# Performance work log

Hardware: AMD Instinct MI355X
Metric: run time of the kernel (lower is better)

The kernel has to match this reference:

```python
import jax, jax.numpy as jnp
import numpy as np

NEG = -1e9  # masked-out (non-edge) additive bias


def _attn_head(seq, bias_mat, W1, a1, b1, a2, b2, W2, bW):
    # seq: [B,N,F]; W1: [F,H]; a1,a2: [H]; W2: [H,K]
    fts = jnp.einsum('bnf,fh->bnh', seq, W1)            # Conv1D(out_sz,1,no bias)
    f1 = jnp.einsum('bnh,h->bn', fts, a1) + b1          # Conv1D(1,1)
    f2 = jnp.einsum('bnh,h->bn', fts, a2) + b2          # Conv1D(1,1)
    logits = f1[:, :, None] + f2[:, None, :]            # [B,N,N] additive attention
    coefs = jax.nn.softmax(jax.nn.leaky_relu(logits, 0.2) + bias_mat, axis=-1)
    vals = jnp.einsum('bnm,bmh->bnh', coefs, fts)       # weighted aggregation
    return jnp.einsum('bnh,hk->bnk', vals, W2) + bW     # bias_add_layer1 (Dense)


def setup_inputs() -> dict:
    B, N, F, H, NH, C = 1, 4096, 512, 64, 8, 40
    key = jax.random.key(0)
    ks = jax.random.split(key, 12)
    seq = jax.random.normal(ks[0], (B, N, F), dtype=jnp.float32)
    adj = jax.random.bernoulli(ks[1], 0.01, (B, N, N)) | jnp.eye(N, dtype=bool)[None]
    bias_mat = jnp.where(adj, 0.0, NEG).astype(jnp.float32)
    s = 0.05
    # 8 stacked first-layer heads (out_sz=H)
    W1 = jax.random.normal(ks[2], (NH, F, H), dtype=jnp.float32) * s
    a1 = jax.random.normal(ks[3], (NH, H), dtype=jnp.float32) * s
    b1 = jnp.zeros((NH,), jnp.float32)
    a2 = jax.random.normal(ks[4], (NH, H), dtype=jnp.float32) * s
    b2 = jnp.zeros((NH,), jnp.float32)
    W2 = jax.random.normal(ks[5], (NH, H, H), dtype=jnp.float32) * s
    bW = jnp.zeros((NH, H), jnp.float32)
    # single output head (out_sz=nb_classes, identity activation)
    Wo1 = jax.random.normal(ks[6], (NH * H, C), dtype=jnp.float32) * s
    ao1 = jax.random.normal(ks[7], (C,), dtype=jnp.float32) * s
    bo1 = jnp.zeros((), jnp.float32)
    ao2 = jax.random.normal(ks[8], (C,), dtype=jnp.float32) * s
    bo2 = jnp.zeros((), jnp.float32)
    Wo2 = jax.random.normal(ks[9], (C, C), dtype=jnp.float32) * s
    bo = jnp.zeros((C,), jnp.float32)
    return dict(seq=seq, bias_mat=bias_mat, W1=W1, a1=a1, b1=b1, a2=a2, b2=b2,
                W2=W2, bW=bW, Wo1=Wo1, ao1=ao1, bo1=bo1, ao2=ao2, bo2=bo2,
                Wo2=Wo2, bo=bo)


def reference(seq, bias_mat, W1, a1, b1, a2, b2, W2, bW,
              Wo1, ao1, bo1, ao2, bo2, Wo2, bo):
    # first layer: 8 heads with elu activation, vmapped over head params
    heads = jax.vmap(
        lambda w1, v1, c1, v2, c2, w2, bw: jax.nn.elu(
            _attn_head(seq, bias_mat, w1, v1, c1, v2, c2, w2, bw))
    )(W1, a1, b1, a2, b2, W2, bW)                        # [NH,B,N,H]
    NH, B, N, H = heads.shape
    h1 = jnp.moveaxis(heads, 0, 2).reshape(B, N, NH * H)  # concat along features
    # output layer: 1 head, identity activation, averaged over n_heads[-1]=1
    out = _attn_head(h1, bias_mat, Wo1, ao1, bo1, ao2, bo2, Wo2, bo)
    return out / 1.0
```

## Files before the change

### kernel.cpp

```cpp
#include <hip/hip_runtime.h>
#include <cstdint>
#include <cstddef>

#define NN 4096
#define FDIM 512
#define HDIM 64
#define NHEAD 8
#define CDIM 40
#define MAXD 256

typedef __attribute__((ext_vector_type(8))) short bf16x8;
typedef __attribute__((ext_vector_type(16))) float f32x16;

__device__ __forceinline__ float wave_max64(float v) {
  for (int o = 32; o; o >>= 1) v = fmaxf(v, __shfl_xor(v, o));
  return v;
}
__device__ __forceinline__ float wave_sum64(float v) {
  for (int o = 32; o; o >>= 1) v += __shfl_xor(v, o);
  return v;
}
__device__ __forceinline__ float readlane_f(float v, int sl) {
  return __uint_as_float((unsigned)__builtin_amdgcn_readlane((int)__float_as_uint(v), sl));
}
__device__ __forceinline__ int readlane_i(int v, int sl) {
  return __builtin_amdgcn_readlane(v, sl);
}
__device__ __forceinline__ unsigned short f2bf(float x) {
  unsigned u = __float_as_uint(x);
  return (unsigned short)((u + 0x7fffu + ((u >> 16) & 1u)) >> 16);
}
__device__ __forceinline__ float bf2f(unsigned short b) {
  return __uint_as_float(((unsigned)b) << 16);
}
__device__ __forceinline__ float lo16f(int u) { return __int_as_float(u << 16); }
__device__ __forceinline__ float hi16f(int u) { return __int_as_float(u & 0xffff0000); }
__device__ __forceinline__ void cvt8(const float4& a, const float4& b,
                                     int4& hi, int4& lo) {
  unsigned short h0 = f2bf(a.x), h1 = f2bf(a.y), h2 = f2bf(a.z), h3 = f2bf(a.w);
  unsigned short h4 = f2bf(b.x), h5 = f2bf(b.y), h6 = f2bf(b.z), h7 = f2bf(b.w);
  hi = make_int4((int)((unsigned)h0 | ((unsigned)h1 << 16)),
                 (int)((unsigned)h2 | ((unsigned)h3 << 16)),
                 (int)((unsigned)h4 | ((unsigned)h5 << 16)),
                 (int)((unsigned)h6 | ((unsigned)h7 << 16)));
  unsigned short l0 = f2bf(a.x - bf2f(h0)), l1 = f2bf(a.y - bf2f(h1));
  unsigned short l2 = f2bf(a.z - bf2f(h2)), l3 = f2bf(a.w - bf2f(h3));
  unsigned short l4 = f2bf(b.x - bf2f(h4)), l5 = f2bf(b.y - bf2f(h5));
  unsigned short l6 = f2bf(b.z - bf2f(h6)), l7 = f2bf(b.w - bf2f(h7));
  lo = make_int4((int)((unsigned)l0 | ((unsigned)l1 << 16)),
                 (int)((unsigned)l2 | ((unsigned)l3 << 16)),
                 (int)((unsigned)l4 | ((unsigned)l5 << 16)),
                 (int)((unsigned)l6 | ((unsigned)l7 << 16)));
}

__global__ __launch_bounds__(256) void k_prep(
    const float* __restrict__ W1, short* __restrict__ Bhi, short* __restrict__ Blo,
    const float* __restrict__ W2, short* __restrict__ W2thi, short* __restrict__ W2tlo,
    const float* __restrict__ Wo1, short* __restrict__ Wo1thi, short* __restrict__ Wo1tlo) {
  __shared__ float T[64][65];
  int bx = blockIdx.x, tid = threadIdx.x;
  if (bx < 64) {
    int h = bx >> 3, kb = bx & 7;
    const float* src = W1 + ((size_t)h * FDIM + kb * 64) * HDIM;
#pragma unroll
    for (int q = 0; q < 4; ++q) {
      int fi = q * 256 + tid, kk = fi >> 4, n4 = fi & 15;
      float4 v = *(const float4*)(src + (size_t)kk * HDIM + n4 * 4);
      T[n4 * 4 + 0][kk] = v.x; T[n4 * 4 + 1][kk] = v.y;
      T[n4 * 4 + 2][kk] = v.z; T[n4 * 4 + 3][kk] = v.w;
    }
    __syncthreads();
#pragma unroll
    for (int q = 0; q < 4; ++q) {
      int fi = q * 256 + tid, n = fi >> 4, k4 = fi & 15;
      float a = T[n][k4 * 4], b = T[n][k4 * 4 + 1];
      float c = T[n][k4 * 4 + 2], d = T[n][k4 * 4 + 3];
      size_t o = ((size_t)h * 64 + n) * FDIM + kb * 64 + k4 * 4;
      unsigned short ha = f2bf(a), hb = f2bf(b), hc = f2bf(c), hd = f2bf(d);
      *(short4*)(Bhi + o) = make_short4((short)ha, (short)hb, (short)hc, (short)hd);
      *(short4*)(Blo + o) = make_short4((short)f2bf(a - bf2f(ha)), (short)f2bf(b - bf2f(hb)),
                                        (short)f2bf(c - bf2f(hc)), (short)f2bf(d - bf2f(hd)));
    }
    return;
  }
  bx -= 64;
  if (bx < 8) {
    int h = bx;
    const float* src = W2 + (size_t)h * HDIM * HDIM;
#pragma unroll
    for (int q = 0; q < 4; ++q) {
      int fi = q * 256 + tid, kk = fi >> 4, n4 = fi & 15;
      float4 v = *(const float4*)(src + (size_t)kk * HDIM + n4 * 4);
      T[n4 * 4 + 0][kk] = v.x; T[n4 * 4 + 1][kk] = v.y;
      T[n4 * 4 + 2][kk] = v.z; T[n4 * 4 + 3][kk] = v.w;
    }
    __syncthreads();
#pragma unroll
    for (int q = 0; q < 4; ++q) {
      int fi = q * 256 + tid, n = fi >> 4, k4 = fi & 15;
      float a = T[n][k4 * 4], b = T[n][k4 * 4 + 1];
      float c = T[n][k4 * 4 + 2], d = T[n][k4 * 4 + 3];
      size_t o = (size_t)h * 4096 + (size_t)n * 64 + k4 * 4;
      unsigned short ha = f2bf(a), hb = f2bf(b), hc = f2bf(c), hd = f2bf(d);
      *(short4*)(W2thi + o) = make_short4((short)ha, (short)hb, (short)hc, (short)hd);
      *(short4*)(W2tlo + o) = make_short4((short)f2bf(a - bf2f(ha)), (short)f2bf(b - bf2f(hb)),
                                          (short)f2bf(c - bf2f(hc)), (short)f2bf(d - bf2f(hd)));
    }
    return;
  }
  bx -= 8;
  {
#pragma unroll
    for (int q = 0; q < 16; ++q) {
      int idx = q * 256 + tid;
      int n = bx * 8 + (idx >> 9), k = idx & 511;
      float v = (n < CDIM) ? Wo1[(size_t)k * CDIM + n] : 0.f;
      unsigned short hv = f2bf(v);
      Wo1thi[(size_t)n * FDIM + k] = (short)hv;
      Wo1tlo[(size_t)n * FDIM + k] = (short)f2bf(v - bf2f(hv));
    }
  }
}

__global__ __launch_bounds__(256) void k_gemm(
    const float* __restrict__ seq,
    const short* __restrict__ Bhi, const short* __restrict__ Blo,
    const float* __restrict__ a1, const float* __restrict__ b1,
    const float* __restrict__ a2, const float* __restrict__ b2,
    short* __restrict__ FTSb, float* __restrict__ F1t, float* __restrict__ F2t,
    const float* __restrict__ bias, int* __restrict__ nbr, int* __restrict__ cnt) {
  __shared__ short AH[4][64][16], AL[4][64][16];
  __shared__ short BH[4][128][16], BL[4][128][16];
  __shared__ int wtot[4];
  const int bx = blockIdx.x;
  const int tid = threadIdx.x, lane = tid & 63, w = tid >> 6;

  if (bx >= 256) {
    int row = bx - 256;
    int wv = w;
    const float4* r = (const float4*)(bias + (size_t)row * NN);
    unsigned mask = 0;
#pragma unroll
    for (int i = 0; i < 4; ++i) {
      float4 v = r[tid * 4 + i];
      mask |= (unsigned)((v.x == 0.f ? 1 : 0) | (v.y == 0.f ? 2 : 0) |
                         (v.z == 0.f ? 4 : 0) | (v.w == 0.f ? 8 : 0)) << (i * 4);
    }
    int c = __popc(mask);
    int pre = c;
#pragma unroll
    for (int o = 1; o < 64; o <<= 1) {
      int u = __shfl_up(pre, o);
      if (lane >= o) pre += u;
    }
    if (lane == 63) wtot[wv] = pre;
    __syncthreads();
    int woff = 0;
#pragma unroll
    for (int ww = 0; ww < 4; ++ww)
      if (ww < wv) woff += wtot[ww];
    int excl = woff + pre - c;
    int* outp = nbr + (size_t)row * MAXD;
    int col0 = tid * 16, k = 0;
#pragma unroll
    for (int i = 0; i < 16; ++i) {
      if ((mask >> i) & 1) {
        int p = excl + k;
        if (p < MAXD) outp[p] = col0 + i;
        ++k;
      }
    }
    if (tid == 0) {
      int total = wtot[0] + wtot[1] + wtot[2] + wtot[3];
      cnt[row] = total < MAXD ? total : MAXD;
    }
    return;
  }

  const int mtile = bx & 63, npair = bx >> 6;
  const int wm = w >> 1, wn = w & 1;
  const int ml = lane & 31, g = lane >> 5, g8 = g * 8;

  f32x16 acc0, acc1;
#pragma unroll
  for (int r = 0; r < 16; ++r) { acc0[r] = 0.f; acc1[r] = 0.f; }

  const short* Bbh = Bhi + (((size_t)npair * 128) << 9);
  const short* Bbl = Blo + (((size_t)npair * 128) << 9);

  const int tn = tid >> 3, k8 = tid & 7;
  const int ks = k8 >> 1, ko = (k8 & 1) * 8;
  const size_t so = ((size_t)tn << 9) + (size_t)k8 * 8;
  const float* As0 = seq + (((size_t)(mtile * 64 + tn)) << 9) + k8 * 8;
  const float* As1 = As0 + ((size_t)32 << 9);

  float4 fa0a, fa0b, fa1a, fa1b;
  int4 rbh0, rbh1, rbh2, rbh3, rbl0, rbl1, rbl2, rbl3;
  {
    fa0a = *(const float4*)(As0);      fa0b = *(const float4*)(As0 + 4);
    fa1a = *(const float4*)(As1);      fa1b = *(const float4*)(As1 + 4);
    rbh0 = *(const int4*)(Bbh + so);              rbl0 = *(const int4*)(Bbl + so);
    rbh1 = *(const int4*)(Bbh + so + (32 << 9));  rbl1 = *(const int4*)(Bbl + so + (32 << 9));
    rbh2 = *(const int4*)(Bbh + so + (64 << 9));  rbl2 = *(const int4*)(Bbl + so + (64 << 9));
    rbh3 = *(const int4*)(Bbh + so + (96 << 9));  rbl3 = *(const int4*)(Bbl + so + (96 << 9));
  }

  const int NCH = FDIM / 64;
  for (int c = 0; c < NCH; ++c) {
    {
      int4 hi0, lo0, hi1, lo1;
      cvt8(fa0a, fa0b, hi0, lo0);
      cvt8(fa1a, fa1b, hi1, lo1);
      *(int4*)&AH[ks][tn][ko] = hi0;       *(int4*)&AL[ks][tn][ko] = lo0;
      *(int4*)&AH[ks][32 + tn][ko] = hi1;  *(int4*)&AL[ks][32 + tn][ko] = lo1;
    }
    *(int4*)&BH[ks][tn][ko] = rbh0;       *(int4*)&BL[ks][tn][ko] = rbl0;
    *(int4*)&BH[ks][32 + tn][ko] = rbh1;  *(int4*)&BL[ks][32 + tn][ko] = rbl1;
    *(int4*)&BH[ks][64 + tn][ko] = rbh2;  *(int4*)&BL[ks][64 + tn][ko] = rbl2;
    *(int4*)&BH[ks][96 + tn][ko] = rbh3;  *(int4*)&BL[ks][96 + tn][ko] = rbl3;
    __syncthreads();
    if (c + 1 < NCH) {
      size_t o = so + (size_t)(c + 1) * 64;
      const float* a0 = As0 + (size_t)(c + 1) * 64;
      const float* a1p = As1 + (size_t)(c + 1) * 64;
      fa0a = *(const float4*)(a0);      fa0b = *(const float4*)(a0 + 4);
      fa1a = *(const float4*)(a1p);     fa1b = *(const float4*)(a1p + 4);
      rbh0 = *(const int4*)(Bbh + o);              rbl0 = *(const int4*)(Bbl + o);
      rbh1 = *(const int4*)(Bbh + o + (32 << 9));  rbl1 = *(const int4*)(Bbl + o + (32 << 9));
      rbh2 = *(const int4*)(Bbh + o + (64 << 9));  rbl2 = *(const int4*)(Bbl + o + (64 << 9));
      rbh3 = *(const int4*)(Bbh + o + (96 << 9));  rbl3 = *(const int4*)(Bbl + o + (96 << 9));
    }
#pragma unroll
    for (int t = 0; t < 4; ++t) {
      bf16x8 ah = *(const bf16x8*)&AH[t][wm * 32 + ml][g8];
      bf16x8 al = *(const bf16x8*)&AL[t][wm * 32 + ml][g8];
      bf16x8 bh0 = *(const bf16x8*)&BH[t][wn * 64 + ml][g8];
      bf16x8 bl0 = *(const bf16x8*)&BL[t][wn * 64 + ml][g8];
      acc0 = __builtin_amdgcn_mfma_f32_32x32x16_bf16(ah, bh0, acc0, 0, 0, 0);
      acc0 = __builtin_amdgcn_mfma_f32_32x32x16_bf16(al, bh0, acc0, 0, 0, 0);
      acc0 = __builtin_amdgcn_mfma_f32_32x32x16_bf16(ah, bl0, acc0, 0, 0, 0);
      bf16x8 bh1 = *(const bf16x8*)&BH[t][wn * 64 + 32 + ml][g8];
      bf16x8 bl1 = *(const bf16x8*)&BL[t][wn * 64 + 32 + ml][g8];
      acc1 = __builtin_amdgcn_mfma_f32_32x32x16_bf16(ah, bh1, acc1, 0, 0, 0);
      acc1 = __builtin_amdgcn_mfma_f32_32x32x16_bf16(al, bh1, acc1, 0, 0, 0);
      acc1 = __builtin_amdgcn_mfma_f32_32x32x16_bf16(ah, bl1, acc1, 0, 0, 0);
    }
    __syncthreads();
  }

  const int h = npair * 2 + wn;
  const float a1lo = a1[h * 64 + ml], a1hi = a1[h * 64 + 32 + ml];
  const float a2lo = a2[h * 64 + ml], a2hi = a2[h * 64 + 32 + ml];
  const float b1h = b1[h], b2h = b2[h];
  const int row0 = mtile * 64 + wm * 32 + 4 * g;
  const int col0 = npair * 128 + wn * 64 + ml;
#pragma unroll
  for (int r = 0; r < 16; ++r) {
    int row = row0 + (r & 3) + 8 * (r >> 2);
    FTSb[(size_t)row * FDIM + col0] = (short)f2bf(acc0[r]);
    FTSb[(size_t)row * FDIM + col0 + 32] = (short)f2bf(acc1[r]);
    float p1 = acc0[r] * a1lo + acc1[r] * a1hi;
    float p2 = acc0[r] * a2lo + acc1[r] * a2hi;
#pragma unroll
    for (int o = 1; o < 32; o <<= 1) {
      p1 += __shfl_xor(p1, o);
      p2 += __shfl_xor(p2, o);
    }
    if (ml == 0) {
      F1t[(size_t)row * 8 + h] = p1 + b1h;
      F2t[(size_t)row * 8 + h] = p2 + b2h;
    }
  }
}

__global__ __launch_bounds__(256) void k_agg1(
    const short* __restrict__ FTSb, const float* __restrict__ F1t,
    const float* __restrict__ F2t, const int* __restrict__ nbr,
    const int* __restrict__ cnt, short* __restrict__ VALShi,
    short* __restrict__ VALSlo) {
  __shared__ float plds[4][MAXD][8];
  int wv = threadIdx.x >> 6, lane = threadIdx.x & 63;
  int i = blockIdx.x * 4 + wv;
  int deg = cnt[i];
  const int* nb = nbr + (size_t)i * MAXD;
  float4 f1a = *(const float4*)(F1t + (size_t)i * 8);
  float4 f1b = *(const float4*)(F1t + (size_t)i * 8 + 4);

  float4 pa[4], pb[4];
  int jreg[4];
  float m0 = -1e30f, m1 = -1e30f, m2 = -1e30f, m3 = -1e30f;
  float m4 = -1e30f, m5 = -1e30f, m6 = -1e30f, m7 = -1e30f;
#pragma unroll
  for (int r = 0; r < 4; ++r) {
    int t = r * 64 + lane;
    jreg[r] = 0;
    pa[r] = make_float4(-1e30f, -1e30f, -1e30f, -1e30f);
    pb[r] = pa[r];
    if (t < deg) {
      int j = nb[t];
      jreg[r] = j;
      float4 f2a = *(const float4*)(F2t + (size_t)j * 8);
      float4 f2b = *(const float4*)(F2t + (size_t)j * 8 + 4);
      float4 xa, xb;
      xa.x = f1a.x + f2a.x; xa.x = xa.x >= 0.f ? xa.x : 0.2f * xa.x;
      xa.y = f1a.y + f2a.y; xa.y = xa.y >= 0.f ? xa.y : 0.2f * xa.y;
      xa.z = f1a.z + f2a.z; xa.z = xa.z >= 0.f ? xa.z : 0.2f * xa.z;
      xa.w = f1a.w + f2a.w; xa.w = xa.w >= 0.f ? xa.w : 0.2f * xa.w;
      xb.x = f1b.x + f2b.x; xb.x = xb.x >= 0.f ? xb.x : 0.2f * xb.x;
      xb.y = f1b.y + f2b.y; xb.y = xb.y >= 0.f ? xb.y : 0.2f * xb.y;
      xb.z = f1b.z + f2b.z; xb.z = xb.z >= 0.f ? xb.z : 0.2f * xb.z;
      xb.w = f1b.w + f2b.w; xb.w = xb.w >= 0.f ? xb.w : 0.2f * xb.w;
      pa[r] = xa; pb[r] = xb;
      m0 = fmaxf(m0, xa.x); m1 = fmaxf(m1, xa.y);
      m2 = fmaxf(m2, xa.z); m3 = fmaxf(m3, xa.w);
      m4 = fmaxf(m4, xb.x); m5 = fmaxf(m5, xb.y);
      m6 = fmaxf(m6, xb.z); m7 = fmaxf(m7, xb.w);
    }
  }
  m0 = wave_max64(m0); m1 = wave_max64(m1); m2 = wave_max64(m2); m3 = wave_max64(m3);
  m4 = wave_max64(m4); m5 = wave_max64(m5); m6 = wave_max64(m6); m7 = wave_max64(m7);
  float s0 = 0.f, s1 = 0.f, s2 = 0.f, s3 = 0.f, s4 = 0.f, s5 = 0.f, s6 = 0.f, s7 = 0.f;
#pragma unroll
  for (int r = 0; r < 4; ++r) {
    int t = r * 64 + lane;
    float4 ea = make_float4(0.f, 0.f, 0.f, 0.f), eb = ea;
    if (t < deg) {
      ea.x = __expf(pa[r].x - m0); ea.y = __expf(pa[r].y - m1);
      ea.z = __expf(pa[r].z - m2); ea.w = __expf(pa[r].w - m3);
      eb.x = __expf(pb[r].x - m4); eb.y = __expf(pb[r].y - m5);
      eb.z = __expf(pb[r].z - m6); eb.w = __expf(pb[r].w - m7);
      *(float4*)&plds[wv][t][0] = ea;
      *(float4*)&plds[wv][t][4] = eb;
    }
    s0 += ea.x; s1 += ea.y; s2 += ea.z; s3 += ea.w;
    s4 += eb.x; s5 += eb.y; s6 += eb.z; s7 += eb.w;
  }
  s0 = wave_sum64(s0); s1 = wave_sum64(s1); s2 = wave_sum64(s2); s3 = wave_sum64(s3);
  s4 = wave_sum64(s4); s5 = wave_sum64(s5); s6 = wave_sum64(s6); s7 = wave_sum64(s7);

  const int q = lane >> 3;
  float sq = (q < 4) ? (q < 2 ? (q == 0 ? s0 : s1) : (q == 2 ? s2 : s3))
                     : (q < 6 ? (q == 4 ? s4 : s5) : (q == 6 ? s6 : s7));
  float inv = 1.f / sq;

  float4 aA = make_float4(0.f, 0.f, 0.f, 0.f), bA = aA;
  float4 aB = aA, bB = aA, aC = aA, bC = aA, aD = aA, bD = aA;
  const size_t lo8 = (size_t)lane * 8;
#pragma unroll
  for (int r = 0; r < 4; ++r) {
    int base = r * 64;
    if (base >= deg) break;
    int lim = deg - base;
    lim = lim < 64 ? lim : 64;
    int sl = 0;
    for (; sl + 4 <= lim; sl += 4) {
      int j0 = readlane_i(jreg[r], sl);
      int j1 = readlane_i(jreg[r], sl + 1);
      int j2 = readlane_i(jreg[r], sl + 2);
      int j3 = readlane_i(jreg[r], sl + 3);
      float w0 = plds[wv][base + sl][q];
      float w1 = plds[wv][base + sl + 1][q];
      float w2 = plds[wv][base + sl + 2][q];
      float w3 = plds[wv][base + sl + 3][q];
      int4 g0 = *(const int4*)(FTSb + (size_t)j0 * FDIM + lo8);
      int4 g1 = *(const int4*)(FTSb + (size_t)j1 * FDIM + lo8);
      int4 g2 = *(const int4*)(FTSb + (size_t)j2 * FDIM + lo8);
      int4 g3 = *(const int4*)(FTSb + (size_t)j3 * FDIM + lo8);
      aA.x += w0 * lo16f(g0.x); aA.y += w0 * hi16f(g0.x);
      aA.z += w0 * lo16f(g0.y); aA.w += w0 * hi16f(g0.y);
      bA.x += w0 * lo16f(g0.z); bA.y += w0 * hi16f(g0.z);
      bA.z += w0 * lo16f(g0.w); bA.w += w0 * hi16f(g0.w);
      aB.x += w1 * lo16f(g1.x); aB.y += w1 * hi16f(g1.x);
      aB.z += w1 * lo16f(g1.y); aB.w += w1 * hi16f(g1.y);
      bB.x += w1 * lo16f(g1.z); bB.y += w1 * hi16f(g1.z);
      bB.z += w1 * lo16f(g1.w); bB.w += w1 * hi16f(g1.w);
      aC.x += w2 * lo16f(g2.x); aC.y += w2 * hi16f(g2.x);
      aC.z += w2 * lo16f(g2.y); aC.w += w2 * hi16f(g2.y);
      bC.x += w2 * lo16f(g2.z); bC.y += w2 * hi16f(g2.z);
      bC.z += w2 * lo16f(g2.w); bC.w += w2 * hi16f(g2.w);
      aD.x += w3 * lo16f(g3.x); aD.y += w3 * hi16f(g3.x);
      aD.z += w3 * lo16f(g3.y); aD.w += w3 * hi16f(g3.y);
      bD.x += w3 * lo16f(g3.z); bD.y += w3 * hi16f(g3.z);
      bD.z += w3 * lo16f(g3.w); bD.w += w3 * hi16f(g3.w);
    }
    for (; sl < lim; ++sl) {
      int j0 = readlane_i(jreg[r], sl);
      float w0 = plds[wv][base + sl][q];
      int4 g0 = *(const int4*)(FTSb + (size_t)j0 * FDIM + lo8);
      aA.x += w0 * lo16f(g0.x); aA.y += w0 * hi16f(g0.x);
      aA.z += w0 * lo16f(g0.y); aA.w += w0 * hi16f(g0.y);
      bA.x += w0 * lo16f(g0.z); bA.y += w0 * hi16f(g0.z);
      bA.z += w0 * lo16f(g0.w); bA.w += w0 * hi16f(g0.w);
    }
  }
  float v0 = (aA.x + aB.x + aC.x + aD.x) * inv;
  float v1 = (aA.y + aB.y + aC.y + aD.y) * inv;
  float v2 = (aA.z + aB.z + aC.z + aD.z) * inv;
  float v3 = (aA.w + aB.w + aC.w + aD.w) * inv;
  float v4 = (bA.x + bB.x + bC.x + bD.x) * inv;
  float v5 = (bA.y + bB.y + bC.y + bD.y) * inv;
  float v6 = (bA.z + bB.z + bC.z + bD.z) * inv;
  float v7 = (bA.w + bB.w + bC.w + bD.w) * inv;
  unsigned short h0 = f2bf(v0), h1 = f2bf(v1), h2 = f2bf(v2), h3 = f2bf(v3);
  unsigned short h4 = f2bf(v4), h5 = f2bf(v5), h6 = f2bf(v6), h7 = f2bf(v7);
  *(int4*)(VALShi + (size_t)i * FDIM + lo8) = make_int4(
      (int)((unsigned)h0 | ((unsigned)h1 << 16)), (int)((unsigned)h2 | ((unsigned)h3 << 16)),
      (int)((unsigned)h4 | ((unsigned)h5 << 16)), (int)((unsigned)h6 | ((unsigned)h7 << 16)));
  unsigned short l0 = f2bf(v0 - bf2f(h0)), l1 = f2bf(v1 - bf2f(h1));
  unsigned short l2 = f2bf(v2 - bf2f(h2)), l3 = f2bf(v3 - bf2f(h3));
  unsigned short l4 = f2bf(v4 - bf2f(h4)), l5 = f2bf(v5 - bf2f(h5));
  unsigned short l6 = f2bf(v6 - bf2f(h6)), l7 = f2bf(v7 - bf2f(h7));
  *(int4*)(VALSlo + (size_t)i * FDIM + lo8) = make_int4(
      (int)((unsigned)l0 | ((unsigned)l1 << 16)), (int)((unsigned)l2 | ((unsigned)l3 << 16)),
      (int)((unsigned)l4 | ((unsigned)l5 << 16)), (int)((unsigned)l6 | ((unsigned)l7 << 16)));
}

__global__ __launch_bounds__(256) void k_tail(
    const short* __restrict__ VALShi, const short* __restrict__ VALSlo,
    const short* __restrict__ W2thi, const short* __restrict__ W2tlo,
    const float* __restrict__ bW,
    const short* __restrict__ Wo1thi, const short* __restrict__ Wo1tlo,
    const float* __restrict__ ao1, const float* __restrict__ bo1s,
    const float* __restrict__ ao2, const float* __restrict__ bo2s,
    float* __restrict__ FTS2, float* __restrict__ F1O, float* __restrict__ F2O) {
  __shared__ short AH[4][64][16], AL[4][64][16];
  __shared__ short BH[4][64][16], BL[4][64][16];
  __shared__ short CH[4][64][16], CL[4][64][16];
  __shared__ short DH[4][64][16], DL[4][64][16];
  __shared__ float p1buf[2][64], p2buf[2][64];
  const int i0 = blockIdx.x * 64;
  const int tid = threadIdx.x, lane = tid & 63, w = tid >> 6;
  const int wm = w >> 1, wn = w & 1;
  const int ml = lane & 31, g = lane >> 5, g8 = g * 8;
  const int tn = tid >> 2, k8 = tid & 3;
  const int colw = wn * 32 + ml;
  const int rowl0 = wm * 32 + 4 * g;

  f32x16 acc2;
#pragma unroll
  for (int r = 0; r < 16; ++r) acc2[r] = 0.f;

  for (int h = 0; h < NHEAD; ++h) {
    {
      const short* pa = VALShi + ((size_t)(i0 + tn) << 9) + h * 64 + k8 * 16;
      const short* pl = VALSlo + ((size_t)(i0 + tn) << 9) + h * 64 + k8 * 16;
      *(int4*)&AH[k8][tn][0] = *(const int4*)pa;
      *(int4*)&AH[k8][tn][8] = *(const int4*)(pa + 8);
      *(int4*)&AL[k8][tn][0] = *(const int4*)pl;
      *(int4*)&AL[k8][tn][8] = *(const int4*)(pl + 8);
      const short* pb  = W2thi + (size_t)h * 4096 + tn * 64 + k8 * 16;
      const short* pbl = W2tlo + (size_t)h * 4096 + tn * 64 + k8 * 16;
      *(int4*)&BH[k8][tn][0] = *(const int4*)pb;
      *(int4*)&BH[k8][tn][8] = *(const int4*)(pb + 8);
      *(int4*)&BL[k8][tn][0] = *(const int4*)pbl;
      *(int4*)&BL[k8][tn][8] = *(const int4*)(pbl + 8);
      const short* pd  = Wo1thi + (size_t)tn * FDIM + h * 64 + k8 * 16;
      const short* pdl = Wo1tlo + (size_t)tn * FDIM + h * 64 + k8 * 16;
      *(int4*)&DH[k8][tn][0] = *(const int4*)pd;
      *(int4*)&DH[k8][tn][8] = *(const int4*)(pd + 8);
      *(int4*)&DL[k8][tn][0] = *(const int4*)pdl;
      *(int4*)&DL[k8][tn][8] = *(const int4*)(pdl + 8);
    }
    __syncthreads();
    f32x16 accw;
#pragma unroll
    for (int r = 0; r < 16; ++r) accw[r] = 0.f;
#pragma unroll
    for (int t = 0; t < 4; ++t) {
      bf16x8 ah = *(const bf16x8*)&AH[t][wm * 32 + ml][g8];
      bf16x8 al = *(const bf16x8*)&AL[t][wm * 32 + ml][g8];
      bf16x8 bh = *(const bf16x8*)&BH[t][wn * 32 + ml][g8];
      bf16x8 bl = *(const bf16x8*)&BL[t][wn * 32 + ml][g8];
      accw = __builtin_amdgcn_mfma_f32_32x32x16_bf16(ah, bh, accw, 0, 0, 0);
      accw = __builtin_amdgcn_mfma_f32_32x32x16_bf16(al, bh, accw, 0, 0, 0);
      accw = __builtin_amdgcn_mfma_f32_32x32x16_bf16(ah, bl, accw, 0, 0, 0);
    }
    const float bwv = bW[h * 64 + colw];
    const int ts = colw >> 4, ss = colw & 15;
#pragma unroll
    for (int r = 0; r < 16; ++r) {
      int rl = rowl0 + (r & 3) + 8 * (r >> 2);
      float v = accw[r] + bwv;
      v = v > 0.f ? v : __expf(v) - 1.f;
      unsigned short hv = f2bf(v);
      CH[ts][rl][ss] = (short)hv;
      CL[ts][rl][ss] = (short)f2bf(v - bf2f(hv));
    }
    __syncthreads();
#pragma unroll
    for (int t = 0; t < 4; ++t) {
      bf16x8 ah = *(const bf16x8*)&CH[t][wm * 32 + ml][g8];
      bf16x8 al = *(const bf16x8*)&CL[t][wm * 32 + ml][g8];
      bf16x8 bh = *(const bf16x8*)&DH[t][wn * 32 + ml][g8];
      bf16x8 bl = *(const bf16x8*)&DL[t][wn * 32 + ml][g8];
      acc2 = __builtin_amdgcn_mfma_f32_32x32x16_bf16(ah, bh, acc2, 0, 0, 0);
      acc2 = __builtin_amdgcn_mfma_f32_32x32x16_bf16(al, bh, acc2, 0, 0, 0);
      acc2 = __builtin_amdgcn_mfma_f32_32x32x16_bf16(ah, bl, acc2, 0, 0, 0);
    }
    __syncthreads();
  }

  const bool act = colw < CDIM;
  const float aov1 = act ? ao1[colw] : 0.f;
  const float aov2 = act ? ao2[colw] : 0.f;
#pragma unroll
  for (int r = 0; r < 16; ++r) {
    int rl = rowl0 + (r & 3) + 8 * (r >> 2);
    float v = acc2[r];
    if (act) FTS2[(size_t)(i0 + rl) * CDIM + colw] = v;
    float p1 = v * aov1, p2 = v * aov2;
#pragma unroll
    for (int o = 1; o < 32; o <<= 1) {
      p1 += __shfl_xor(p1, o);
      p2 += __shfl_xor(p2, o);
    }
    if (ml == 0) {
      p1buf[wn][rl] = p1;
      p2buf[wn][rl] = p2;
    }
  }
  __syncthreads();
  if (tid < 64) {
    F1O[i0 + tid] = p1buf[0][tid] + p1buf[1][tid] + bo1s[0];
    F2O[i0 + tid] = p2buf[0][tid] + p2buf[1][tid] + bo2s[0];
  }
}

__global__ __launch_bounds__(256) void k_agg2(
    const float* __restrict__ FTS2, const float* __restrict__ F1O,
    const float* __restrict__ F2O, const int* __restrict__ nbr,
    const int* __restrict__ cnt, const float* __restrict__ Wo2,
    const float* __restrict__ bo, float* __restrict__ out) {
  int i = blockIdx.x * 4 + (threadIdx.x >> 6);
  int lane = threadIdx.x & 63;
  int deg = cnt[i];
  const int* nb = nbr + (size_t)i * MAXD;
  float f1i = F1O[i];

  int jreg[4];
  float p[4];
  float m = -1e30f;
#pragma unroll
  for (int r = 0; r < 4; ++r) { jreg[r] = 0; p[r] = -1e30f; }
#pragma unroll
  for (int r = 0; r < 4; ++r) {
    int t = r * 64 + lane;
    if (t < deg) {
      int j = nb[t];
      jreg[r] = j;
      float x = f1i + F2O[j];
      x = x >= 0.f ? x : 0.2f * x;
      p[r] = x;
      m = fmaxf(m, x);
    }
  }
  m = wave_max64(m);
  float s = 0.f;
#pragma unroll
  for (int r = 0; r < 4; ++r) {
    int t = r * 64 + lane;
    float e = (t < deg) ? __expf(p[r] - m) : 0.f;
    p[r] = e;
    s += e;
  }
  s = wave_sum64(s);

  const bool act = lane < CDIM;
  float accA = 0.f, accB = 0.f, accC = 0.f, accD = 0.f;
#pragma unroll
  for (int r = 0; r < 4; ++r) {
    int base = r * 64;
    if (base >= deg) break;
    int lim = deg - base;
    lim = lim < 64 ? lim : 64;
    int sl = 0;
    for (; sl + 4 <= lim; sl += 4) {
      float w0 = readlane_f(p[r], sl);
      float w1 = readlane_f(p[r], sl + 1);
      float w2 = readlane_f(p[r], sl + 2);
      float w3 = readlane_f(p[r], sl + 3);
      int j0 = readlane_i(jreg[r], sl);
      int j1 = readlane_i(jreg[r], sl + 1);
      int j2 = readlane_i(jreg[r], sl + 2);
      int j3 = readlane_i(jreg[r], sl + 3);
      float f0 = act ? FTS2[(size_t)j0 * CDIM + lane] : 0.f;
      float f1 = act ? FTS2[(size_t)j1 * CDIM + lane] : 0.f;
      float f2 = act ? FTS2[(size_t)j2 * CDIM + lane] : 0.f;
      float f3 = act ? FTS2[(size_t)j3 * CDIM + lane] : 0.f;
      accA += w0 * f0;
      accB += w1 * f1;
      accC += w2 * f2;
      accD += w3 * f3;
    }
    for (; sl < lim; ++sl) {
      float w0 = readlane_f(p[r], sl);
      int j0 = readlane_i(jreg[r], sl);
      float f0 = act ? FTS2[(size_t)j0 * CDIM + lane] : 0.f;
      accA += w0 * f0;
    }
  }
  float v = (accA + accB + accC + accD) / s;

  float o = act ? bo[lane] : 0.f;
  for (int kk = 0; kk < CDIM; ++kk) {
    float w = readlane_f(v, kk);
    float b = act ? Wo2[kk * CDIM + lane] : 0.f;
    o += w * b;
  }
  if (act) out[(size_t)i * CDIM + lane] = o;
}

extern "C" void kernel_launch(void* const* d_in, const int* in_sizes, int n_in,
                              void* d_out, int out_size, void* d_ws, size_t ws_size,
                              hipStream_t stream) {
  const float* seq  = (const float*)d_in[0];
  const float* bias = (const float*)d_in[1];
  const float* W1   = (const float*)d_in[2];
  const float* a1   = (const float*)d_in[3];
  const float* b1   = (const float*)d_in[4];
  const float* a2   = (const float*)d_in[5];
  const float* b2   = (const float*)d_in[6];
  const float* W2   = (const float*)d_in[7];
  const float* bW   = (const float*)d_in[8];
  const float* Wo1  = (const float*)d_in[9];
  const float* ao1  = (const float*)d_in[10];
  const float* bo1  = (const float*)d_in[11];
  const float* ao2  = (const float*)d_in[12];
  const float* bo2  = (const float*)d_in[13];
  const float* Wo2  = (const float*)d_in[14];
  const float* bo   = (const float*)d_in[15];
  float* out = (float*)d_out;

  float* ws    = (float*)d_ws;
  float* F1t   = ws;
  float* F2t   = F1t  + (size_t)NN * NHEAD;
  float* FTS2  = F2t  + (size_t)NN * NHEAD;
  float* F1O   = FTS2 + (size_t)NN * CDIM;
  float* F2O   = F1O  + NN;
  short* FTSb  = (short*)(F2O + NN);
  short* Bhi   = FTSb + (size_t)NN * FDIM;
  short* Blo   = Bhi + (size_t)NHEAD * HDIM * FDIM;
  short* VALShi= Blo + (size_t)NHEAD * HDIM * FDIM;
  short* VALSlo= VALShi + (size_t)NN * FDIM;
  short* W2thi = VALSlo + (size_t)NN * FDIM;
  short* W2tlo = W2thi + (size_t)NHEAD * HDIM * HDIM;
  short* Wo1thi= W2tlo + (size_t)NHEAD * HDIM * HDIM;
  short* Wo1tlo= Wo1thi + (size_t)64 * FDIM;
  int*   nbr   = (int*)(Wo1tlo + (size_t)64 * FDIM);
  int*   cnt   = nbr + (size_t)NN * MAXD;

  k_prep<<<64 + 8 + 8, 256, 0, stream>>>(
      W1, Bhi, Blo, W2, W2thi, W2tlo, Wo1, Wo1thi, Wo1tlo);
  k_gemm<<<256 + NN, 256, 0, stream>>>(
      seq, Bhi, Blo, a1, b1, a2, b2, FTSb, F1t, F2t, bias, nbr, cnt);
  k_agg1<<<NN / 4, 256, 0, stream>>>(FTSb, F1t, F2t, nbr, cnt, VALShi, VALSlo);
  k_tail<<<NN / 64, 256, 0, stream>>>(VALShi, VALSlo, W2thi, W2tlo, bW,
                                      Wo1thi, Wo1tlo, ao1, bo1, ao2, bo2,
                                      FTS2, F1O, F2O);
  k_agg2<<<NN / 4, 256, 0, stream>>>(FTS2, F1O, F2O, nbr, cnt, Wo2, bo, out);
}
```

Baseline: 85.00 us.

## Split k_tail head reduction across two blocks and sum partials in k_agg2

```diff
diff --git a/kernel.cpp b/kernel.cpp
--- a/kernel.cpp
+++ b/kernel.cpp
@@ -420,15 +420,16 @@
     const short* __restrict__ W2thi, const short* __restrict__ W2tlo,
     const float* __restrict__ bW,
     const short* __restrict__ Wo1thi, const short* __restrict__ Wo1tlo,
-    const float* __restrict__ ao1, const float* __restrict__ bo1s,
-    const float* __restrict__ ao2, const float* __restrict__ bo2s,
+    const float* __restrict__ ao1, const float* __restrict__ ao2,
     float* __restrict__ FTS2, float* __restrict__ F1O, float* __restrict__ F2O) {
   __shared__ short AH[4][64][16], AL[4][64][16];
   __shared__ short BH[4][64][16], BL[4][64][16];
   __shared__ short CH[4][64][16], CL[4][64][16];
   __shared__ short DH[4][64][16], DL[4][64][16];
   __shared__ float p1buf[2][64], p2buf[2][64];
-  const int i0 = blockIdx.x * 64;
+  const int bx = blockIdx.x;
+  const int i0 = (bx >> 1) * 64;
+  const int hg = bx & 1;
   const int tid = threadIdx.x, lane = tid & 63, w = tid >> 6;
   const int wm = w >> 1, wn = w & 1;
   const int ml = lane & 31, g = lane >> 5, g8 = g * 8;
@@ -440,7 +441,8 @@
 #pragma unroll
   for (int r = 0; r < 16; ++r) acc2[r] = 0.f;
 
-  for (int h = 0; h < NHEAD; ++h) {
+  for (int hh = 0; hh < 4; ++hh) {
+    const int h = hg * 4 + hh;
     {
       const short* pa = VALShi + ((size_t)(i0 + tn) << 9) + h * 64 + k8 * 16;
       const short* pl = VALSlo + ((size_t)(i0 + tn) << 9) + h * 64 + k8 * 16;
@@ -500,6 +502,7 @@
     __syncthreads();
   }
 
+  float* FTS2p = FTS2 + (size_t)hg * NN * CDIM;
   const bool act = colw < CDIM;
   const float aov1 = act ? ao1[colw] : 0.f;
   const float aov2 = act ? ao2[colw] : 0.f;
@@ -507,7 +510,7 @@
   for (int r = 0; r < 16; ++r) {
     int rl = rowl0 + (r & 3) + 8 * (r >> 2);
     float v = acc2[r];
-    if (act) FTS2[(size_t)(i0 + rl) * CDIM + colw] = v;
+    if (act) FTS2p[(size_t)(i0 + rl) * CDIM + colw] = v;
     float p1 = v * aov1, p2 = v * aov2;
 #pragma unroll
     for (int o = 1; o < 32; o <<= 1) {
@@ -521,8 +524,8 @@
   }
   __syncthreads();
   if (tid < 64) {
-    F1O[i0 + tid] = p1buf[0][tid] + p1buf[1][tid] + bo1s[0];
-    F2O[i0 + tid] = p2buf[0][tid] + p2buf[1][tid] + bo2s[0];
+    F1O[(size_t)hg * NN + i0 + tid] = p1buf[0][tid] + p1buf[1][tid];
+    F2O[(size_t)hg * NN + i0 + tid] = p2buf[0][tid] + p2buf[1][tid];
   }
 }
 
@@ -530,12 +533,15 @@
     const float* __restrict__ FTS2, const float* __restrict__ F1O,
     const float* __restrict__ F2O, const int* __restrict__ nbr,
     const int* __restrict__ cnt, const float* __restrict__ Wo2,
-    const float* __restrict__ bo, float* __restrict__ out) {
+    const float* __restrict__ bo, const float* __restrict__ bo1s,
+    const float* __restrict__ bo2s, float* __restrict__ out) {
   int i = blockIdx.x * 4 + (threadIdx.x >> 6);
   int lane = threadIdx.x & 63;
   int deg = cnt[i];
   const int* nb = nbr + (size_t)i * MAXD;
-  float f1i = F1O[i];
+  const float* F2Ob = F2O + NN;
+  const float* FTS2b = FTS2 + (size_t)NN * CDIM;
+  float f1ib = F1O[i] + F1O[NN + i] + bo1s[0] + bo2s[0];
 
   int jreg[4];
   float p[4];
@@ -548,7 +554,7 @@
     if (t < deg) {
       int j = nb[t];
       jreg[r] = j;
-      float x = f1i + F2O[j];
+      float x = f1ib + F2O[j] + F2Ob[j];
       x = x >= 0.f ? x : 0.2f * x;
       p[r] = x;
       m = fmaxf(m, x);
@@ -583,10 +589,10 @@
       int j1 = readlane_i(jreg[r], sl + 1);
       int j2 = readlane_i(jreg[r], sl + 2);
       int j3 = readlane_i(jreg[r], sl + 3);
-      float f0 = act ? FTS2[(size_t)j0 * CDIM + lane] : 0.f;
-      float f1 = act ? FTS2[(size_t)j1 * CDIM + lane] : 0.f;
-      float f2 = act ? FTS2[(size_t)j2 * CDIM + lane] : 0.f;
-      float f3 = act ? FTS2[(size_t)j3 * CDIM + lane] : 0.f;
+      float f0 = act ? (FTS2[(size_t)j0 * CDIM + lane] + FTS2b[(size_t)j0 * CDIM + lane]) : 0.f;
+      float f1 = act ? (FTS2[(size_t)j1 * CDIM + lane] + FTS2b[(size_t)j1 * CDIM + lane]) : 0.f;
+      float f2 = act ? (FTS2[(size_t)j2 * CDIM + lane] + FTS2b[(size_t)j2 * CDIM + lane]) : 0.f;
+      float f3 = act ? (FTS2[(size_t)j3 * CDIM + lane] + FTS2b[(size_t)j3 * CDIM + lane]) : 0.f;
       accA += w0 * f0;
       accB += w1 * f1;
       accC += w2 * f2;
@@ -595,7 +601,7 @@
     for (; sl < lim; ++sl) {
       float w0 = readlane_f(p[r], sl);
       int j0 = readlane_i(jreg[r], sl);
-      float f0 = act ? FTS2[(size_t)j0 * CDIM + lane] : 0.f;
+      float f0 = act ? (FTS2[(size_t)j0 * CDIM + lane] + FTS2b[(size_t)j0 * CDIM + lane]) : 0.f;
       accA += w0 * f0;
     }
   }
@@ -635,9 +641,9 @@
   float* F1t   = ws;
   float* F2t   = F1t  + (size_t)NN * NHEAD;
   float* FTS2  = F2t  + (size_t)NN * NHEAD;
-  float* F1O   = FTS2 + (size_t)NN * CDIM;
-  float* F2O   = F1O  + NN;
-  short* FTSb  = (short*)(F2O + NN);
+  float* F1O   = FTS2 + (size_t)2 * NN * CDIM;
+  float* F2O   = F1O  + 2 * NN;
+  short* FTSb  = (short*)(F2O + 2 * NN);
   short* Bhi   = FTSb + (size_t)NN * FDIM;
   short* Blo   = Bhi + (size_t)NHEAD * HDIM * FDIM;
   short* VALShi= Blo + (size_t)NHEAD * HDIM * FDIM;
@@ -654,8 +660,9 @@
   k_gemm<<<256 + NN, 256, 0, stream>>>(
       seq, Bhi, Blo, a1, b1, a2, b2, FTSb, F1t, F2t, bias, nbr, cnt);
   k_agg1<<<NN / 4, 256, 0, stream>>>(FTSb, F1t, F2t, nbr, cnt, VALShi, VALSlo);
-  k_tail<<<NN / 64, 256, 0, stream>>>(VALShi, VALSlo, W2thi, W2tlo, bW,
-                                      Wo1thi, Wo1tlo, ao1, bo1, ao2, bo2,
-                                      FTS2, F1O, F2O);
-  k_agg2<<<NN / 4, 256, 0, stream>>>(FTS2, F1O, F2O, nbr, cnt, Wo2, bo, out);
-}
+  k_tail<<<NN / 64 * 2, 256, 0, stream>>>(VALShi, VALSlo, W2thi, W2tlo, bW,
+                                          Wo1thi, Wo1tlo, ao1, ao2,
+                                          FTS2, F1O, F2O);
+  k_agg2<<<NN / 4, 256, 0, stream>>>(FTS2, F1O, F2O, nbr, cnt, Wo2, bo,
+                                     bo1, bo2, out);
+}
```

Result: faster. 83.11 us, median of 2 (-2.2%).
